# Kernel tuning notes

Hardware: AMD Instinct MI355X
Metric: run time of the kernel (lower is better)

The kernel has to match this reference:

```python
import jax, jax.numpy as jnp
import numpy as np

N = 2048      # number of ROIs
C = 1024      # in_channels == inter_channels
G = 16        # groups
D = C // G    # per-group dim = 64


def _bbox_overlaps(b1, b2):
    # mmdet-1.x IoU with +1 pixel convention; b1:(N,4), b2:(M,4)
    area1 = (b1[:, 2] - b1[:, 0] + 1) * (b1[:, 3] - b1[:, 1] + 1)  # (N,)
    area2 = (b2[:, 2] - b2[:, 0] + 1) * (b2[:, 3] - b2[:, 1] + 1)  # (M,)
    lt = jnp.maximum(b1[:, None, :2], b2[None, :, :2])             # (N,M,2)
    rb = jnp.minimum(b1[:, None, 2:], b2[None, :, 2:])             # (N,M,2)
    wh = jnp.clip(rb - lt + 1, 0)
    inter = wh[..., 0] * wh[..., 1]                                # (N,M)
    return inter / (area1[:, None] + area2[None, :] - inter)


def setup_inputs() -> dict:
    key = jax.random.key(0)
    ks = jax.random.split(key, 9)
    in_x = jax.random.normal(ks[0], (N, C), dtype=jnp.float32)
    # valid boxes: [batch_idx, x1, y1, x2, y2]
    xy = jax.random.uniform(ks[1], (N, 2), minval=0.0, maxval=800.0)
    wh = jax.random.uniform(ks[2], (N, 2), minval=8.0, maxval=200.0)
    rois = jnp.concatenate([jnp.zeros((N, 1)), xy, xy + wh], axis=1).astype(jnp.float32)
    s = 1.0 / np.sqrt(C)
    W0 = jax.random.normal(ks[3], (C, C), dtype=jnp.float32) * s
    b0 = jnp.zeros((C,), dtype=jnp.float32)
    W1 = jax.random.normal(ks[4], (C, C), dtype=jnp.float32) * s
    b1 = jnp.zeros((C,), dtype=jnp.float32)
    # grouped 1x1 conv: per group maps C channels -> D channels
    Wout = jax.random.normal(ks[5], (G, D, C), dtype=jnp.float32) * s
    bout = jnp.zeros((C,), dtype=jnp.float32)
    return {"in_x": in_x, "rois": rois, "W0": W0, "b0": b0, "W1": W1,
            "b1": b1, "Wout": Wout, "bout": bout}


def reference(in_x, rois, W0, b0, W1, b1, Wout, bout):
    # self-attention path: in_ref_x = in_x, ref_rois = rois
    # embed convs are pre-activation (relu -> 1x1 conv), shared for x and ref_x
    def embed(v):
        v = jax.nn.relu(v) @ W0.T + b0
        v = jax.nn.relu(v) @ W1.T + b1
        return v
    x = embed(in_x)                      # (N, C)
    ref_x = x                            # shared convs, same input
    xg = x.reshape(N, G, D)
    rg = ref_x.reshape(N, G, D)
    scores = jnp.einsum('ngd,mgd->ngm', xg, rg) / jnp.sqrt(jnp.float32(D))  # (N,G,N)
    ious = _bbox_overlaps(rois[:, 1:], rois[:, 1:])                          # (N,N)
    scores = scores + jnp.log(ious[:, None, :] + 1e-6)
    attn = jax.nn.softmax(scores, axis=2)                                    # (N,G,N)
    y = jnp.einsum('ngm,mc->ngc', attn, in_x)                                # (N,G,C)
    out = jnp.einsum('ngc,goc->ngo', y, Wout).reshape(N, C) + bout           # (N,C)
    return out
```

## Files before the change

### kernel.cpp

```cpp
#include <hip/hip_runtime.h>
#include <math.h>

constexpr int NROI = 2048;
constexpr int CDIM = 1024;
constexpr int NG   = 16;
constexpr int DH   = 64;

typedef __attribute__((ext_vector_type(8))) short short8;
typedef __attribute__((ext_vector_type(4))) float floatx4;

#define MFMA_BF16(a, b, c) __builtin_amdgcn_mfma_f32_16x16x32_bf16((a), (b), (c), 0, 0, 0)

__device__ __forceinline__ short f2bf(float f) {
  unsigned u = __float_as_uint(f);
  unsigned r = 0x7fffu + ((u >> 16) & 1u);
  return (short)((u + r) >> 16);
}
__device__ __forceinline__ float bf2f(unsigned short u) {
  return __uint_as_float(((unsigned)u) << 16);
}
__device__ __forceinline__ unsigned pack2(float a, float b) {
  return (unsigned)(unsigned short)f2bf(a) | ((unsigned)(unsigned short)f2bf(b) << 16);
}

typedef __attribute__((address_space(1))) void GV;
typedef __attribute__((address_space(3))) void LV;
__device__ __forceinline__ void gl2lds16(const void* g, void* l) {
  __builtin_amdgcn_global_load_lds((GV*)g, (LV*)l, 16, 0, 0);
}

__device__ __forceinline__ short8 brelu(short8 v) {
  union { short8 s; unsigned u[4]; } x; x.s = v;
#pragma unroll
  for (int i = 0; i < 4; ++i) {
    unsigned m = (x.u[i] >> 15) & 0x10001u;
    x.u[i] &= ~(m * 0xFFFFu);
  }
  return x.s;
}

__device__ __forceinline__ int keypos(int k) {
  return (k & ~31) | (((k >> 2) & 3) << 3) | (((k >> 4) & 1) << 2);
}

__global__ __launch_bounds__(256) void convert_kernel(
    const float* __restrict__ in_x, const float* __restrict__ W0,
    const float* __restrict__ W1, const float* __restrict__ Wout,
    short* __restrict__ xin_b, short* __restrict__ W0b,
    short* __restrict__ W1b, short* __restrict__ Woutb)
{
  const int i = blockIdx.x * 256 + threadIdx.x;
  {
    const float4 v = ((const float4*)in_x)[i];
    uint2 u; u.x = pack2(v.x, v.y); u.y = pack2(v.z, v.w);
    ((uint2*)xin_b)[i] = u;
  }
  if (i < 262144) {
    float4 v = ((const float4*)W0)[i];
    uint2 u; u.x = pack2(v.x, v.y); u.y = pack2(v.z, v.w);
    ((uint2*)W0b)[i] = u;
    v = ((const float4*)W1)[i];
    u.x = pack2(v.x, v.y); u.y = pack2(v.z, v.w);
    ((uint2*)W1b)[i] = u;
    v = ((const float4*)Wout)[i];
    u.x = pack2(v.x, v.y); u.y = pack2(v.z, v.w);
    ((uint2*)Woutb)[i] = u;
  }
}

__global__ __launch_bounds__(256) void iou4_kernel(const float* __restrict__ rois,
                                                   unsigned short* __restrict__ biasb)
{
  const int q  = blockIdx.y;
  const int k0 = (blockIdx.x * 256 + threadIdx.x) * 4;
  const float qx1 = rois[q * 5 + 1], qy1 = rois[q * 5 + 2];
  const float qx2 = rois[q * 5 + 3], qy2 = rois[q * 5 + 4];
  const float qa = (qx2 - qx1 + 1.f) * (qy2 - qy1 + 1.f);
  float v[4];
#pragma unroll
  for (int j = 0; j < 4; ++j) {
    const int k = k0 + j;
    const float kx1 = rois[k * 5 + 1], ky1 = rois[k * 5 + 2];
    const float kx2 = rois[k * 5 + 3], ky2 = rois[k * 5 + 4];
    const float ka = (kx2 - kx1 + 1.f) * (ky2 - ky1 + 1.f);
    float iw = fminf(qx2, kx2) - fmaxf(qx1, kx1) + 1.f;
    float ih = fminf(qy2, ky2) - fmaxf(qy1, ky1) + 1.f;
    iw = fmaxf(iw, 0.f); ih = fmaxf(ih, 0.f);
    const float inter = iw * ih;
    v[j] = inter * __builtin_amdgcn_rcpf(qa + ka - inter) + 1e-6f;
  }
  uint2 u; u.x = pack2(v[0], v[1]); u.y = pack2(v[2], v[3]);
  *(uint2*)&biasb[(size_t)q * NROI + keypos(k0)] = u;
}

template <int FUSED>
__global__ __launch_bounds__(256, 4) void gemm64(
    const short* __restrict__ A, const short* __restrict__ Ba,
    const short* __restrict__ Bb, const float* __restrict__ bias,
    short* __restrict__ outRM, short* __restrict__ outTR)
{
  __shared__ short As[2][8 * 512];
  __shared__ short Bs[2][8 * 512];
  const int t = threadIdx.x, w = t >> 6, lane = t & 63;
  const int wm = w >> 1, wn = w & 1;
  const int row0 = blockIdx.y * 64;
  bool isW0; int col0; const short* B;
  if (FUSED) {
    isW0 = blockIdx.x < 16;
    col0 = (blockIdx.x & 15) * 64;
    B = isW0 ? Ba : Bb;
  } else {
    isW0 = true; col0 = blockIdx.x * 64; B = Ba;
  }
  const bool doRelu = FUSED ? isW0 : true;
  const int rlo = lane & 15, khi = (lane >> 4) * 8;

  floatx4 acc[2][2];
#pragma unroll
  for (int i = 0; i < 2; ++i)
#pragma unroll
    for (int j = 0; j < 2; ++j) acc[i][j] = (floatx4){0.f, 0.f, 0.f, 0.f};

#pragma unroll
  for (int kh = 0; kh < 2; ++kh) {
    const int f = w * 2 + kh;
    gl2lds16(A + (size_t)(row0 + w * 16 + rlo) * CDIM + kh * 32 + khi, &As[0][f * 512]);
    gl2lds16(B + (size_t)(col0 + w * 16 + rlo) * CDIM + kh * 32 + khi, &Bs[0][f * 512]);
  }
  __syncthreads();

  for (int it = 0; it < 16; ++it) {
    const int p = it & 1;
    if (it < 15) {
      const int k1 = (it + 1) * 64;
#pragma unroll
      for (int kh = 0; kh < 2; ++kh) {
        const int f = w * 2 + kh;
        gl2lds16(A + (size_t)(row0 + w * 16 + rlo) * CDIM + k1 + kh * 32 + khi,
                 &As[1 - p][f * 512]);
        gl2lds16(B + (size_t)(col0 + w * 16 + rlo) * CDIM + k1 + kh * 32 + khi,
                 &Bs[1 - p][f * 512]);
      }
    }
#pragma unroll
    for (int kh = 0; kh < 2; ++kh) {
      short8 a[2], bf[2];
#pragma unroll
      for (int i = 0; i < 2; ++i) {
        a[i] = *(const short8*)&As[p][((wm * 2 + i) * 2 + kh) * 512 + lane * 8];
        if (doRelu) a[i] = brelu(a[i]);
      }
#pragma unroll
      for (int j = 0; j < 2; ++j)
        bf[j] = *(const short8*)&Bs[p][((wn * 2 + j) * 2 + kh) * 512 + lane * 8];
#pragma unroll
      for (int i = 0; i < 2; ++i)
#pragma unroll
        for (int j = 0; j < 2; ++j)
          acc[i][j] = MFMA_BF16(a[i], bf[j], acc[i][j]);
    }
    __syncthreads();
  }

  const int colL = lane & 15, qq = lane >> 4;
  if (!FUSED || isW0) {
    float bj[2];
    bj[0] = bias[col0 + wn * 32 + colL];
    bj[1] = bias[col0 + wn * 32 + 16 + colL];
#pragma unroll
    for (int i = 0; i < 2; ++i)
#pragma unroll
      for (int j = 0; j < 2; ++j)
#pragma unroll
        for (int r = 0; r < 4; ++r) {
          const int row = row0 + wm * 32 + i * 16 + qq * 4 + r;
          const int cc  = col0 + wn * 32 + j * 16 + colL;
          outRM[(size_t)row * CDIM + cc] = f2bf(acc[i][j][r] + bj[j]);
        }
  } else {
#pragma unroll
    for (int i = 0; i < 2; ++i)
#pragma unroll
      for (int j = 0; j < 2; ++j) {
        unsigned long long u =
            (unsigned long long)pack2(acc[i][j][0], acc[i][j][1]) |
            ((unsigned long long)pack2(acc[i][j][2], acc[i][j][3]) << 32);
        const int cc  = col0 + wn * 32 + j * 16 + colL;
        const int row = row0 + wm * 32 + i * 16 + qq * 4;
        *(unsigned long long*)&outTR[(size_t)cc * NROI + keypos(row)] = u;
      }
  }
}

__global__ __launch_bounds__(1024, 4) void attn_bias(
    const short* __restrict__ Xb,
    const short* __restrict__ ZTb,
    const unsigned short* __restrict__ biasb,
    const float* __restrict__ bout,
    float* __restrict__ Out)
{
  const int g  = blockIdx.y;
  const int n0 = blockIdx.x * 128;
  const int t  = threadIdx.x;
  const int w    = t >> 6;
  const int half = w >> 3;
  const int wq   = w & 7;
  const int lane = t & 63;
  const int col  = lane & 15;
  const int qq   = lane >> 4;
  const int t16 = (wq >> 1) * 16;
  const int h32 = (wq & 1) * 32;
  const int rlo = lane & 15, khi = qq * 8;

  __shared__ short Kf[2][2][4096];
  __shared__ short Vf[2][2][4096];

  const size_t qoff = (size_t)(n0 + wq * 16 + col) * CDIM + g * DH;
  const short8 qf0 = *(const short8*)(Xb + qoff + qq * 8);
  const short8 qf1 = *(const short8*)(Xb + qoff + 32 + qq * 8);

  floatx4 oc[4];
#pragma unroll
  for (int dt = 0; dt < 4; ++dt) oc[dt] = (floatx4){0.f, 0.f, 0.f, 0.f};
  float lsum = 0.f;

  const int mbase = half * 1024;
  gl2lds16(Xb + (size_t)(mbase + t16 + rlo) * CDIM + g * DH + h32 + khi,
           &Kf[half][0][wq * 512]);
  gl2lds16(ZTb + (size_t)(g * DH + t16 + rlo) * NROI + mbase + h32 + khi,
           &Vf[half][0][wq * 512]);
  __syncthreads();

  const unsigned short* bq =
      biasb + (size_t)(n0 + wq * 16 + col) * NROI + mbase + qq * 8;

  for (int it = 0; it < 16; ++it) {
    const int p  = it & 1;
    const int m0 = mbase + it * 64;

    union { short8 s[2]; unsigned short h[16]; } BU;
    BU.s[0] = *(const short8*)(bq + it * 64);
    BU.s[1] = *(const short8*)(bq + it * 64 + 32);

    if (it + 1 < 16) {
      const int m1 = m0 + 64;
      gl2lds16(Xb + (size_t)(m1 + t16 + rlo) * CDIM + g * DH + h32 + khi,
               &Kf[half][1 - p][wq * 512]);
      gl2lds16(ZTb + (size_t)(g * DH + t16 + rlo) * NROI + m1 + h32 + khi,
               &Vf[half][1 - p][wq * 512]);
    }

    float e[4][4];
#pragma unroll
    for (int ct = 0; ct < 4; ++ct) {
      const short8 k0 = *(const short8*)&Kf[half][p][(ct * 2 + 0) * 512 + lane * 8];
      const short8 k1 = *(const short8*)&Kf[half][p][(ct * 2 + 1) * 512 + lane * 8];
      floatx4 z4 = (floatx4){0.f, 0.f, 0.f, 0.f};
      z4 = MFMA_BF16(k0, qf0, z4);
      z4 = MFMA_BF16(k1, qf1, z4);
#pragma unroll
      for (int r = 0; r < 4; ++r) e[ct][r] = z4[r];
    }

#pragma unroll
    for (int ct = 0; ct < 4; ++ct)
#pragma unroll
      for (int r = 0; r < 4; ++r) {
        const float pv = __expf(e[ct][r] * 0.125f) * bf2f(BU.h[ct * 4 + r]);
        e[ct][r] = pv;
        lsum += pv;
      }

    union { short8 s; unsigned u[4]; } U0, U1;
#pragma unroll
    for (int j = 0; j < 2; ++j) {
      U0.u[j * 2 + 0] = pack2(e[j][0], e[j][1]);
      U0.u[j * 2 + 1] = pack2(e[j][2], e[j][3]);
      U1.u[j * 2 + 0] = pack2(e[j + 2][0], e[j + 2][1]);
      U1.u[j * 2 + 1] = pack2(e[j + 2][2], e[j + 2][3]);
    }

#pragma unroll
    for (int dt = 0; dt < 4; ++dt) {
      const short8 v0 = *(const short8*)&Vf[half][p][(dt * 2 + 0) * 512 + lane * 8];
      const short8 v1 = *(const short8*)&Vf[half][p][(dt * 2 + 1) * 512 + lane * 8];
      oc[dt] = MFMA_BF16(U0.s, v0, oc[dt]);
      oc[dt] = MFMA_BF16(U1.s, v1, oc[dt]);
    }
    __syncthreads();
  }

  float s = lsum;
  s += __shfl_xor(s, 16);
  s += __shfl_xor(s, 32);

  float* ocb = (float*)&Kf[0][0][0];
  float* lsb = (float*)&Vf[0][0][0];
  const int cbase = (wq * 64 + lane) * 16;
  if (half) {
#pragma unroll
    for (int dt = 0; dt < 4; ++dt)
#pragma unroll
      for (int r = 0; r < 4; ++r) ocb[cbase + dt * 4 + r] = oc[dt][r];
    lsb[wq * 64 + lane] = s;
  }
  __syncthreads();
  if (!half) {
    s += lsb[wq * 64 + lane];
    float ls[4];
#pragma unroll
    for (int r = 0; r < 4; ++r)
      ls[r] = __shfl(s, (qq << 4) | (qq * 4 + r));
#pragma unroll
    for (int dt = 0; dt < 4; ++dt) {
      const float bo = bout[g * DH + dt * 16 + col];
#pragma unroll
      for (int r = 0; r < 4; ++r)
        Out[(size_t)(n0 + wq * 16 + qq * 4 + r) * CDIM + g * DH + dt * 16 + col] =
            (oc[dt][r] + ocb[cbase + dt * 4 + r]) / ls[r] + bo;
    }
  }
}

extern "C" void kernel_launch(void* const* d_in, const int* in_sizes, int n_in,
                              void* d_out, int out_size, void* d_ws, size_t ws_size,
                              hipStream_t stream) {
  const float* in_x = (const float*)d_in[0];
  const float* rois = (const float*)d_in[1];
  const float* W0   = (const float*)d_in[2];
  const float* b0   = (const float*)d_in[3];
  const float* W1   = (const float*)d_in[4];
  const float* b1   = (const float*)d_in[5];
  const float* Wout = (const float*)d_in[6];
  const float* bout = (const float*)d_in[7];
  char* w8 = (char*)d_ws;

  short* xin_b = (short*)w8;
  short* W0b   = (short*)(w8 + ((size_t)4 << 20));
  short* W1b   = (short*)(w8 + ((size_t)6 << 20));
  short* Woutb = (short*)(w8 + ((size_t)8 << 20));
  short* zT    = (short*)(w8 + ((size_t)10 << 20));
  unsigned short* biasb = (unsigned short*)(w8 + ((size_t)14 << 20));
  short* xb  = xin_b;
  short* t0b = (short*)d_out;

  convert_kernel<<<2048, 256, 0, stream>>>(in_x, W0, W1, Wout,
                                           xin_b, W0b, W1b, Woutb);
  iou4_kernel<<<dim3(2, NROI), 256, 0, stream>>>(rois, biasb);
  gemm64<1><<<dim3(32, 32), 256, 0, stream>>>(xin_b, W0b, Woutb, b0, t0b, zT);
  gemm64<0><<<dim3(16, 32), 256, 0, stream>>>(t0b, W1b, nullptr, b1, xb, nullptr);
  attn_bias<<<dim3(NROI / 128, NG), 1024, 0, stream>>>(xb, zT, biasb, bout,
                                                       (float*)d_out);
}
```

Baseline: 183.9 us.

## Shrink attention blocks to 64 queries with XCD-aware group mapping and cheaper math

```diff
diff --git a/kernel.cpp b/kernel.cpp
--- a/kernel.cpp
+++ b/kernel.cpp
@@ -21,6 +21,20 @@
 }
 __device__ __forceinline__ unsigned pack2(float a, float b) {
   return (unsigned)(unsigned short)f2bf(a) | ((unsigned)(unsigned short)f2bf(b) << 16);
+}
+
+__device__ __forceinline__ unsigned cvtpk_bf16(float lo, float hi) {
+  unsigned r;
+  asm("v_cvt_pk_bf16_f32 %0, %1, %2" : "=v"(r) : "v"(lo), "v"(hi));
+  return r;
+}
+
+__device__ __forceinline__ float fexp2(float x) {
+#if __has_builtin(__builtin_amdgcn_exp2f)
+  return __builtin_amdgcn_exp2f(x);
+#else
+  return __expf(x * 0.69314718056f);
+#endif
 }
 
 typedef __attribute__((address_space(1))) void GV;
@@ -192,25 +206,27 @@
   }
 }
 
-__global__ __launch_bounds__(1024, 4) void attn_bias(
+__global__ __launch_bounds__(512, 4) void attn_bias(
     const short* __restrict__ Xb,
     const short* __restrict__ ZTb,
     const unsigned short* __restrict__ biasb,
     const float* __restrict__ bout,
     float* __restrict__ Out)
 {
-  const int g  = blockIdx.y;
-  const int n0 = blockIdx.x * 128;
-  const int t  = threadIdx.x;
+  const int lin  = blockIdx.x + 32 * blockIdx.y;
+  const int xcd  = lin & 7;
+  const int slot = lin >> 3;
+  const int g    = 2 * xcd + (slot >> 5);
+  const int n0   = (slot & 31) * 64;
+
+  const int t    = threadIdx.x;
   const int w    = t >> 6;
-  const int half = w >> 3;
-  const int wq   = w & 7;
+  const int half = w >> 2;
+  const int wq   = w & 3;
   const int lane = t & 63;
   const int col  = lane & 15;
   const int qq   = lane >> 4;
-  const int t16 = (wq >> 1) * 16;
-  const int h32 = (wq & 1) * 32;
-  const int rlo = lane & 15, khi = qq * 8;
+  const int rlo  = col, khi = qq * 8;
 
   __shared__ short Kf[2][2][4096];
   __shared__ short Vf[2][2][4096];
@@ -225,10 +241,13 @@
   float lsum = 0.f;
 
   const int mbase = half * 1024;
-  gl2lds16(Xb + (size_t)(mbase + t16 + rlo) * CDIM + g * DH + h32 + khi,
-           &Kf[half][0][wq * 512]);
-  gl2lds16(ZTb + (size_t)(g * DH + t16 + rlo) * NROI + mbase + h32 + khi,
-           &Vf[half][0][wq * 512]);
+#pragma unroll
+  for (int kh = 0; kh < 2; ++kh) {
+    gl2lds16(Xb + (size_t)(mbase + wq * 16 + rlo) * CDIM + g * DH + kh * 32 + khi,
+             &Kf[half][0][(wq * 2 + kh) * 512]);
+    gl2lds16(ZTb + (size_t)(g * DH + wq * 16 + rlo) * NROI + mbase + kh * 32 + khi,
+             &Vf[half][0][(wq * 2 + kh) * 512]);
+  }
   __syncthreads();
 
   const unsigned short* bq =
@@ -244,13 +263,17 @@
 
     if (it + 1 < 16) {
       const int m1 = m0 + 64;
-      gl2lds16(Xb + (size_t)(m1 + t16 + rlo) * CDIM + g * DH + h32 + khi,
-               &Kf[half][1 - p][wq * 512]);
-      gl2lds16(ZTb + (size_t)(g * DH + t16 + rlo) * NROI + m1 + h32 + khi,
-               &Vf[half][1 - p][wq * 512]);
+#pragma unroll
+      for (int kh = 0; kh < 2; ++kh) {
+        gl2lds16(Xb + (size_t)(m1 + wq * 16 + rlo) * CDIM + g * DH + kh * 32 + khi,
+                 &Kf[half][1 - p][(wq * 2 + kh) * 512]);
+        gl2lds16(ZTb + (size_t)(g * DH + wq * 16 + rlo) * NROI + m1 + kh * 32 + khi,
+                 &Vf[half][1 - p][(wq * 2 + kh) * 512]);
+      }
     }
 
     float e[4][4];
+    __builtin_amdgcn_s_setprio(1);
 #pragma unroll
     for (int ct = 0; ct < 4; ++ct) {
       const short8 k0 = *(const short8*)&Kf[half][p][(ct * 2 + 0) * 512 + lane * 8];
@@ -261,12 +284,13 @@
 #pragma unroll
       for (int r = 0; r < 4; ++r) e[ct][r] = z4[r];
     }
+    __builtin_amdgcn_s_setprio(0);
 
 #pragma unroll
     for (int ct = 0; ct < 4; ++ct)
 #pragma unroll
       for (int r = 0; r < 4; ++r) {
-        const float pv = __expf(e[ct][r] * 0.125f) * bf2f(BU.h[ct * 4 + r]);
+        const float pv = fexp2(e[ct][r] * 0.18033688011f) * bf2f(BU.h[ct * 4 + r]);
         e[ct][r] = pv;
         lsum += pv;
       }
@@ -274,12 +298,13 @@
     union { short8 s; unsigned u[4]; } U0, U1;
 #pragma unroll
     for (int j = 0; j < 2; ++j) {
-      U0.u[j * 2 + 0] = pack2(e[j][0], e[j][1]);
-      U0.u[j * 2 + 1] = pack2(e[j][2], e[j][3]);
-      U1.u[j * 2 + 0] = pack2(e[j + 2][0], e[j + 2][1]);
-      U1.u[j * 2 + 1] = pack2(e[j + 2][2], e[j + 2][3]);
-    }
-
+      U0.u[j * 2 + 0] = cvtpk_bf16(e[j][0], e[j][1]);
+      U0.u[j * 2 + 1] = cvtpk_bf16(e[j][2], e[j][3]);
+      U1.u[j * 2 + 0] = cvtpk_bf16(e[j + 2][0], e[j + 2][1]);
+      U1.u[j * 2 + 1] = cvtpk_bf16(e[j + 2][2], e[j + 2][3]);
+    }
+
+    __builtin_amdgcn_s_setprio(1);
 #pragma unroll
     for (int dt = 0; dt < 4; ++dt) {
       const short8 v0 = *(const short8*)&Vf[half][p][(dt * 2 + 0) * 512 + lane * 8];
@@ -287,6 +312,7 @@
       oc[dt] = MFMA_BF16(U0.s, v0, oc[dt]);
       oc[dt] = MFMA_BF16(U1.s, v1, oc[dt]);
     }
+    __builtin_amdgcn_s_setprio(0);
     __syncthreads();
   }
 
@@ -307,17 +333,20 @@
   __syncthreads();
   if (!half) {
     s += lsb[wq * 64 + lane];
-    float ls[4];
+    float ls[4], rinv[4];
 #pragma unroll
     for (int r = 0; r < 4; ++r)
       ls[r] = __shfl(s, (qq << 4) | (qq * 4 + r));
 #pragma unroll
+    for (int r = 0; r < 4; ++r)
+      rinv[r] = __builtin_amdgcn_rcpf(ls[r]);
+#pragma unroll
     for (int dt = 0; dt < 4; ++dt) {
       const float bo = bout[g * DH + dt * 16 + col];
 #pragma unroll
       for (int r = 0; r < 4; ++r)
         Out[(size_t)(n0 + wq * 16 + qq * 4 + r) * CDIM + g * DH + dt * 16 + col] =
-            (oc[dt][r] + ocb[cbase + dt * 4 + r]) / ls[r] + bo;
+            (oc[dt][r] + ocb[cbase + dt * 4 + r]) * rinv[r] + bo;
     }
   }
 }
@@ -349,6 +378,6 @@
   iou4_kernel<<<dim3(2, NROI), 256, 0, stream>>>(rois, biasb);
   gemm64<1><<<dim3(32, 32), 256, 0, stream>>>(xin_b, W0b, Woutb, b0, t0b, zT);
   gemm64<0><<<dim3(16, 32), 256, 0, stream>>>(t0b, W1b, nullptr, b1, xb, nullptr);
-  attn_bias<<<dim3(NROI / 128, NG), 1024, 0, stream>>>(xb, zT, biasb, bout,
-                                                       (float*)d_out);
-}
+  attn_bias<<<dim3(32, NG), 512, 0, stream>>>(xb, zT, biasb, bout,
+                                              (float*)d_out);
+}
```

Result: slower. 191.0 us (+3.9%).
